# Performance work log

Hardware: AMD Instinct MI355X
Metric: run time of the kernel (lower is better)

## Reference

```python
import jax, jax.numpy as jnp
import numpy as np


def setup_inputs() -> dict:
    key = jax.random.key(0)
    ks = jax.random.split(key, 6)
    b, t, s, qu, vu, d = 8, 64, 512, 512, 512, 512
    return {
        "query": jax.random.normal(ks[0], (b, t, qu), jnp.float32),
        "value": jax.random.normal(ks[1], (b, s, vu), jnp.float32),
        "mask": jax.random.randint(ks[2], (b, s), 0, 2).astype(bool),
        "W1_w": jax.random.normal(ks[3], (qu, d), jnp.float32) * (1.0 / np.sqrt(qu)),
        "W1_b": jnp.zeros((d,), jnp.float32),
        "W2_w": jax.random.normal(ks[4], (vu, d), jnp.float32) * (1.0 / np.sqrt(vu)),
        "W2_b": jnp.zeros((d,), jnp.float32),
        "scale": jax.random.normal(ks[5], (d,), jnp.float32) * 0.05,
    }


def reference(query, value, mask, W1_w, W1_b, W2_w, W2_b, scale):
    # Dense projections
    q = jnp.einsum('btq,qd->btd', query, W1_w) + W1_b   # [b,t,d]
    k = jnp.einsum('bsv,vd->bsd', value, W2_w) + W2_b   # [b,s,d]
    # Additive (Bahdanau) score with learned scale vector (Keras use_scale=True)
    # scores[b,t,s] = sum_d scale[d] * tanh(q[b,t,d] + k[b,s,d])
    scores = jnp.einsum('btsd,d->bts', jnp.tanh(q[:, :, None, :] + k[:, None, :, :]), scale)
    # Mask over source positions (value mask); query mask is all-ones (no-op)
    scores = jnp.where(mask[:, None, :], scores, jnp.float32(-1e9))
    attention_weights = jax.nn.softmax(scores, axis=-1)   # [b,t,s]
    context_vector = jnp.einsum('bts,bsv->btv', attention_weights, value)  # [b,t,vu]
    return context_vector, attention_weights
```

## Files before the change

### kernel.cpp

```cpp
#include <hip/hip_runtime.h>
#include <hip/hip_bf16.h>
#include <hip/hip_fp16.h>

#define B_  8
#define T_  64
#define S_  512
#define D_  512

#define QN (512 * 512)
#define KN (4096 * 512)

#define TLOG2E 2.8853900817779268f
#define LOG2E  1.4426950408889634f

typedef __attribute__((ext_vector_type(8))) short bf16x8;
typedef __attribute__((ext_vector_type(4))) float f32x4;

__device__ __forceinline__ unsigned int pk2(float a, float b) {
    float2 f; f.x = a; f.y = b;
    __hip_bfloat162 h = __float22bfloat162_rn(f);
    return *(unsigned int*)&h;
}
__device__ __forceinline__ unsigned int pkh(float a, float b) {
    __half2 h = __floats2half2_rn(a, b);
    return *(unsigned int*)&h;
}
__device__ __forceinline__ float2 up2(unsigned int u) {
    __half2 h = *(__half2*)&u;
    return __half22float2(h);
}

__global__ __launch_bounds__(256) void mfma_gemm(
    const float* __restrict__ query, const float* __restrict__ value,
    const float* __restrict__ W1, const float* __restrict__ W2,
    const float* __restrict__ b1, const float* __restrict__ b2,
    float* __restrict__ qproj, unsigned short* __restrict__ kTb,
    unsigned short* __restrict__ vh)
{
    __shared__ __align__(16) unsigned short Ab[2][64][72];
    __shared__ __align__(16) unsigned short Bs[2][64][72];

    const int x = blockIdx.x;
    const int tid  = threadIdx.x;

    if (x >= 576) {
        const int c = x - 576;
        const float* src = value + (size_t)c * 128 * 512;
        unsigned short* dst = vh + (size_t)c * 128 * 512;
#pragma unroll 4
        for (int i = 0; i < 64; ++i) {
            const int f = i * 256 + tid;
            float4 v4 = *(const float4*)(src + (size_t)f * 4);
            uint2 o; o.x = pkh(v4.x, v4.y); o.y = pkh(v4.z, v4.w);
            *(uint2*)(dst + (size_t)f * 4) = o;
        }
        return;
    }

    const float *A, *W;
    int tm, tn;
    bool isq;
    if (x < 512) {
        tm = (x & 7) * 8 + ((x >> 3) & 7);
        tn = x >> 6;
        A = value; W = W2; isq = false;
    } else {
        int r = x - 512;
        tm = r >> 3; tn = r & 7;
        A = query; W = W1; isq = true;
    }

    const int lane = tid & 63;
    const int wid  = tid >> 6;
    const int wm = (wid & 1) * 32, wn = (wid >> 1) * 32;
    const int fm = lane & 15, fq = lane >> 4;

    f32x4 acc00 = {0.f, 0.f, 0.f, 0.f};
    f32x4 acc01 = acc00, acc10 = acc00, acc11 = acc00;

    const int ar = tid >> 2;
    const int kc = (tid & 3) * 16;
    const float* Ag = A + (size_t)(tm * 64 + ar) * 512 + kc;
    const int c0 = (tid & 15) * 4;
    const int kp = (tid >> 4) * 2;
    const float* Wg = W + (size_t)kp * 512 + tn * 64 + c0;

    float4 av0, av1, av2, av3;
    float4 wv0, wv1, wv2, wv3;

#define LOADT(KOFF) do {                                                      \
        av0 = *(const float4*)(Ag + (KOFF));                                  \
        av1 = *(const float4*)(Ag + (KOFF) + 4);                              \
        av2 = *(const float4*)(Ag + (KOFF) + 8);                              \
        av3 = *(const float4*)(Ag + (KOFF) + 12);                             \
        wv0 = *(const float4*)(Wg + (size_t)(KOFF) * 512);                    \
        wv1 = *(const float4*)(Wg + (size_t)(KOFF) * 512 + 512);              \
        wv2 = *(const float4*)(Wg + (size_t)((KOFF) + 32) * 512);             \
        wv3 = *(const float4*)(Wg + (size_t)((KOFF) + 32) * 512 + 512);       \
    } while (0)

#define STAGE(BUF) do {                                                       \
        uint4 p0, p1;                                                         \
        p0.x = pk2(av0.x, av0.y); p0.y = pk2(av0.z, av0.w);                   \
        p0.z = pk2(av1.x, av1.y); p0.w = pk2(av1.z, av1.w);                   \
        p1.x = pk2(av2.x, av2.y); p1.y = pk2(av2.z, av2.w);                   \
        p1.z = pk2(av3.x, av3.y); p1.w = pk2(av3.z, av3.w);                   \
        *(uint4*)&Ab[BUF][ar][kc]     = p0;                                   \
        *(uint4*)&Ab[BUF][ar][kc + 8] = p1;                                   \
        *(unsigned int*)&Bs[BUF][c0 + 0][kp]      = pk2(wv0.x, wv1.x);        \
        *(unsigned int*)&Bs[BUF][c0 + 1][kp]      = pk2(wv0.y, wv1.y);        \
        *(unsigned int*)&Bs[BUF][c0 + 2][kp]      = pk2(wv0.z, wv1.z);        \
        *(unsigned int*)&Bs[BUF][c0 + 3][kp]      = pk2(wv0.w, wv1.w);        \
        *(unsigned int*)&Bs[BUF][c0 + 0][kp + 32] = pk2(wv2.x, wv3.x);        \
        *(unsigned int*)&Bs[BUF][c0 + 1][kp + 32] = pk2(wv2.y, wv3.y);        \
        *(unsigned int*)&Bs[BUF][c0 + 2][kp + 32] = pk2(wv2.z, wv3.z);        \
        *(unsigned int*)&Bs[BUF][c0 + 3][kp + 32] = pk2(wv2.w, wv3.w);        \
    } while (0)

    LOADT(0);
    STAGE(0);
    LOADT(64);
    __syncthreads();

    for (int i = 0; i < 8; ++i) {
        const int cur = i & 1, nxt = cur ^ 1;
        bf16x8 a0, a1, b0, b1v;
#pragma unroll
        for (int kk = 0; kk < 64; kk += 32) {
            a0  = *(const bf16x8*)&Ab[cur][wm + fm][kk + fq * 8];
            a1  = *(const bf16x8*)&Ab[cur][wm + 16 + fm][kk + fq * 8];
            b0  = *(const bf16x8*)&Bs[cur][wn + fm][kk + fq * 8];
            b1v = *(const bf16x8*)&Bs[cur][wn + 16 + fm][kk + fq * 8];
            acc00 = __builtin_amdgcn_mfma_f32_16x16x32_bf16(a0, b0,  acc00, 0, 0, 0);
            acc01 = __builtin_amdgcn_mfma_f32_16x16x32_bf16(a0, b1v, acc01, 0, 0, 0);
            acc10 = __builtin_amdgcn_mfma_f32_16x16x32_bf16(a1, b0,  acc10, 0, 0, 0);
            acc11 = __builtin_amdgcn_mfma_f32_16x16x32_bf16(a1, b1v, acc11, 0, 0, 0);
        }
        if (i < 7) {
            STAGE(nxt);
            const int kn = ((i + 2) & 7) * 64;
            LOADT(kn);
        }
        __syncthreads();
    }
#undef STAGE
#undef LOADT

    const int n0 = tn * 64 + wn + fm;
    const int n1 = n0 + 16;
    const int m0 = tm * 64 + wm + fq * 4;
    if (isq) {
        float bias0 = b1[n0] + b2[n0];
        float bias1 = b1[n1] + b2[n1];
#pragma unroll
        for (int r = 0; r < 4; ++r) {
            qproj[(size_t)(m0 + r) * 512 + n0]      = (acc00[r] + bias0) * TLOG2E;
            qproj[(size_t)(m0 + r) * 512 + n1]      = (acc01[r] + bias1) * TLOG2E;
            qproj[(size_t)(m0 + 16 + r) * 512 + n0] = (acc10[r] + bias0) * TLOG2E;
            qproj[(size_t)(m0 + 16 + r) * 512 + n1] = (acc11[r] + bias1) * TLOG2E;
        }
    } else {
        const int bb = m0 >> 9;
        const int sl = m0 & 511;
        unsigned short* kb = kTb + (size_t)(bb * 512) * 512;
#define EX2(V) __builtin_amdgcn_exp2f((V) * TLOG2E)
        uint2 o;
        o.x = pkh(EX2(acc00[0]), EX2(acc00[1]));
        o.y = pkh(EX2(acc00[2]), EX2(acc00[3]));
        *(uint2*)(kb + (size_t)n0 * 512 + sl) = o;
        o.x = pkh(EX2(acc10[0]), EX2(acc10[1]));
        o.y = pkh(EX2(acc10[2]), EX2(acc10[3]));
        *(uint2*)(kb + (size_t)n0 * 512 + sl + 16) = o;
        o.x = pkh(EX2(acc01[0]), EX2(acc01[1]));
        o.y = pkh(EX2(acc01[2]), EX2(acc01[3]));
        *(uint2*)(kb + (size_t)n1 * 512 + sl) = o;
        o.x = pkh(EX2(acc11[0]), EX2(acc11[1]));
        o.y = pkh(EX2(acc11[2]), EX2(acc11[3]));
        *(uint2*)(kb + (size_t)n1 * 512 + sl + 16) = o;
#undef EX2
    }
}

__global__ __launch_bounds__(1024) void fused_attn(
    const float* __restrict__ qproj, const unsigned short* __restrict__ kTb,
    const int*   __restrict__ mask,  const float* __restrict__ scale,
    const unsigned short* __restrict__ vh,
    float* __restrict__ ctx, float* __restrict__ attn)
{
    const int blk = blockIdx.x;
    const int b  = blk & 7;
    const int tp = blk >> 3;
    const size_t row0 = (size_t)(b * T_ + tp * 2);

    __shared__ __align__(16) float q0A[512];
    __shared__ __align__(16) float dA[512];
    __shared__ __align__(16) float cA[512];
    __shared__ __align__(16) float4 pex[4][256];
    __shared__ __align__(16) float4 part[2][8][128];
    __shared__ __align__(16) float2 wc[8][64];
    __shared__ int  sidc[8][64];
    __shared__ int  cntA[8];
    __shared__ float2 red2[16];

    const int tid  = threadIdx.x;
    const int lane = tid & 63;
    const int wid  = tid >> 6;

    if (tid < 512) {
        float q0v = qproj[row0 * D_ + tid];
        float q1v = qproj[(row0 + 1) * D_ + tid];
        q0A[tid] = __builtin_amdgcn_exp2f(q0v);
        dA[tid]  = __builtin_amdgcn_exp2f(q1v - q0v);
        cA[tid]  = scale[tid];
    }
    __syncthreads();

    const int sp  = tid & 255;
    const int dq  = tid >> 8;
    const int dlo = dq * 128;
    const unsigned short* kb = kTb + ((size_t)(b * 512 + dlo)) * 512 + sp * 2;

    float p00 = 0.f, p10 = 0.f, p01 = 0.f, p11 = 0.f;

    unsigned int nf0 = *(const unsigned int*)(kb);
    unsigned int nf1 = *(const unsigned int*)(kb + 512);
    unsigned int nf2 = *(const unsigned int*)(kb + 1024);
    unsigned int nf3 = *(const unsigned int*)(kb + 1536);

#define SC2(KU, EQ, DV, CV) do {                                              \
        float2 ek = up2(KU);                                                  \
        float e0 = (EQ) * ek.x;                                               \
        float ra = __builtin_amdgcn_rcpf(e0 + 1.0f);                          \
        float rb = __builtin_amdgcn_rcpf(fmaf(e0, (DV), 1.0f));               \
        p00 = fmaf((CV), ra, p00); p10 = fmaf((CV), rb, p10);                 \
        float e1 = (EQ) * ek.y;                                               \
        float rc = __builtin_amdgcn_rcpf(e1 + 1.0f);                          \
        float rd = __builtin_amdgcn_rcpf(fmaf(e1, (DV), 1.0f));               \
        p01 = fmaf((CV), rc, p01); p11 = fmaf((CV), rd, p11);                 \
    } while (0)

    for (int g = 0; g < 32; ++g) {
        unsigned int kf0 = nf0, kf1 = nf1, kf2 = nf2, kf3 = nf3;
        const unsigned short* nb = kb + (size_t)(((g + 1) & 31) * 4) * 512;
        nf0 = *(const unsigned int*)(nb);
        nf1 = *(const unsigned int*)(nb + 512);
        nf2 = *(const unsigned int*)(nb + 1024);
        nf3 = *(const unsigned int*)(nb + 1536);
        const int d0 = dlo + g * 4;
        float4 q4 = *(const float4*)&q0A[d0];
        float4 dl = *(const float4*)&dA[d0];
        float4 c4 = *(const float4*)&cA[d0];
        SC2(kf0, q4.x, dl.x, c4.x);
        SC2(kf1, q4.y, dl.y, c4.y);
        SC2(kf2, q4.z, dl.z, c4.z);
        SC2(kf3, q4.w, dl.w, c4.w);
    }
#undef SC2

    {
        float4 pq; pq.x = p00; pq.y = p10; pq.z = p01; pq.w = p11;
        pex[dq][sp] = pq;
    }
    __syncthreads();

    float e0 = 0.f, e1 = 0.f;
    int   m = 0, rank = 0;
    if (tid < 512) {
        const int s = tid;
        const int s2 = s >> 1;
        const bool odd = (s & 1) != 0;
        float4 r0 = pex[0][s2], r1 = pex[1][s2];
        float4 r2 = pex[2][s2], r3 = pex[3][s2];
        float pt0 = odd ? ((r0.z + r1.z) + (r2.z + r3.z))
                        : ((r0.x + r1.x) + (r2.x + r3.x));
        float pt1 = odd ? ((r0.w + r1.w) + (r2.w + r3.w))
                        : ((r0.y + r1.y) + (r2.y + r3.y));
        m = mask[b * S_ + s];
        if (m) {
            e0 = __builtin_amdgcn_exp2f(-TLOG2E * pt0);
            e1 = __builtin_amdgcn_exp2f(-TLOG2E * pt1);
        }
        unsigned long long bal = __ballot(m != 0);
        rank = __popcll(bal & ((1ull << lane) - 1ull));
        if (lane == 0) cntA[wid] = (int)__popcll(bal);
        if (m) sidc[wid][rank] = lane;
        float2 sm; sm.x = e0; sm.y = e1;
#pragma unroll
        for (int off = 32; off >= 1; off >>= 1) {
            sm.x += __shfl_xor(sm.x, off);
            sm.y += __shfl_xor(sm.y, off);
        }
        if (lane == 0) red2[wid] = sm;
    }
    __syncthreads();

    if (tid < 512) {
        const int s = tid;
        float2 SS = red2[0];
#pragma unroll
        for (int i = 1; i < 8; ++i) {
            SS.x += red2[i].x;
            SS.y += red2[i].y;
        }
        const float w0 = e0 * __builtin_amdgcn_rcpf(SS.x);
        const float w1 = e1 * __builtin_amdgcn_rcpf(SS.y);
        if (m) {
            float2 wpair; wpair.x = w0; wpair.y = w1;
            wc[wid][rank] = wpair;
        }
        attn[row0 * S_ + s]       = w0;
        attn[(row0 + 1) * S_ + s] = w1;
    }
    __syncthreads();

    const int g  = tid >> 7;
    const int v4 = tid & 127;
    const unsigned short* vbase = vh + ((size_t)(b * S_) + g * 64) * D_ + v4 * 4;
    float4 a0; a0.x = 0.f; a0.y = 0.f; a0.z = 0.f; a0.w = 0.f;
    float4 a1 = a0;

    const int cnt = cntA[g];
    float2 w0r, w1r; uint2 u0r, u1r;
    w0r.x = 0.f; w0r.y = 0.f; w1r = w0r;
    u0r.x = 0u; u0r.y = 0u; u1r = u0r;
    if (0 < cnt) {
        int so = sidc[g][0]; w0r = wc[g][0];
        u0r = *(const uint2*)(vbase + (size_t)so * D_);
    }
    if (1 < cnt) {
        int so = sidc[g][1]; w1r = wc[g][1];
        u1r = *(const uint2*)(vbase + (size_t)so * D_);
    }
    for (int r = 0; r < cnt; ++r) {
        float2 w = w0r; uint2 u = u0r;
        w0r = w1r; u0r = u1r;
        if (r + 2 < cnt) {
            int so = sidc[g][r + 2]; w1r = wc[g][r + 2];
            u1r = *(const uint2*)(vbase + (size_t)so * D_);
        }
        float2 lo = up2(u.x), hi = up2(u.y);
        a0.x = fmaf(w.x, lo.x, a0.x); a0.y = fmaf(w.x, lo.y, a0.y);
        a0.z = fmaf(w.x, hi.x, a0.z); a0.w = fmaf(w.x, hi.y, a0.w);
        a1.x = fmaf(w.y, lo.x, a1.x); a1.y = fmaf(w.y, lo.y, a1.y);
        a1.z = fmaf(w.y, hi.x, a1.z); a1.w = fmaf(w.y, hi.y, a1.w);
    }
    part[0][g][v4] = a0;
    part[1][g][v4] = a1;
    __syncthreads();
    if (tid < 256) {
        const int t = tid >> 7, v = tid & 127;
        float4 o; o.x = 0.f; o.y = 0.f; o.z = 0.f; o.w = 0.f;
#pragma unroll
        for (int gg = 0; gg < 8; ++gg) {
            float4 p = part[t][gg][v];
            o.x += p.x; o.y += p.y; o.z += p.z; o.w += p.w;
        }
        *(float4*)(ctx + (row0 + t) * D_ + v * 4) = o;
    }
}

extern "C" void kernel_launch(void* const* d_in, const int* in_sizes, int n_in,
                              void* d_out, int out_size, void* d_ws, size_t ws_size,
                              hipStream_t stream) {
    const float* query = (const float*)d_in[0];
    const float* value = (const float*)d_in[1];
    const int*   mask  = (const int*)  d_in[2];
    const float* W1w   = (const float*)d_in[3];
    const float* W1b   = (const float*)d_in[4];
    const float* W2w   = (const float*)d_in[5];
    const float* W2b   = (const float*)d_in[6];
    const float* scale = (const float*)d_in[7];

    float* ctx  = (float*)d_out;
    float* attn = (float*)d_out + (size_t)B_ * T_ * D_;

    float* qproj = (float*)d_ws;
    unsigned short* kTb = (unsigned short*)(qproj + (size_t)QN);
    unsigned short* vh  = kTb + (size_t)KN;

    mfma_gemm<<<608, 256, 0, stream>>>(query, value, W1w, W2w, W1b, W2b,
                                       qproj, kTb, vh);
    fused_attn<<<256, 1024, 0, stream>>>(qproj, kTb, mask, scale, vh,
                                         ctx, attn);
}
```

Measured before the change: 125.5 us.

## Compact masked source positions before score computation to skip masked tanh work

The kernel now builds a compacted list of unmasked source indices at the start of each block and evaluates the additive tanh score only for those positions. Masked positions previously paid the full D-loop cost before being discarded. Work per block drops roughly in proportion to the mask density. In exchange, K loads become scattered 16-bit gathers instead of coalesced 32-bit pair loads. The context reduction is also rebalanced so the compacted entries are split evenly across wave groups, and masked attention outputs are written as zero directly.

```diff
diff --git a/kernel.cpp b/kernel.cpp
--- a/kernel.cpp
+++ b/kernel.cpp
@@ -197,93 +197,119 @@
     __shared__ __align__(16) float cA[512];
     __shared__ __align__(16) float4 pex[4][256];
     __shared__ __align__(16) float4 part[2][8][128];
-    __shared__ __align__(16) float2 wc[8][64];
-    __shared__ int  sidc[8][64];
-    __shared__ int  cntA[8];
+    __shared__ __align__(16) float2 wc[512];
+    __shared__ int  sidc[512];
+    __shared__ int  mA[512];
+    __shared__ int  wcnt[8];
+    __shared__ int  cntS;
     __shared__ float2 red2[16];
 
     const int tid  = threadIdx.x;
     const int lane = tid & 63;
     const int wid  = tid >> 6;
 
+    int m = 0, rank = 0;
     if (tid < 512) {
         float q0v = qproj[row0 * D_ + tid];
         float q1v = qproj[(row0 + 1) * D_ + tid];
         q0A[tid] = __builtin_amdgcn_exp2f(q0v);
         dA[tid]  = __builtin_amdgcn_exp2f(q1v - q0v);
         cA[tid]  = scale[tid];
-    }
-    __syncthreads();
-
-    const int sp  = tid & 255;
+        m = mask[b * S_ + tid];
+        mA[tid] = m;
+        unsigned long long bal = __ballot(m != 0);
+        rank = __popcll(bal & ((1ull << lane) - 1ull));
+        if (lane == 0) wcnt[wid] = (int)__popcll(bal);
+    }
+    __syncthreads();
+    if (tid < 512) {
+        int off = 0;
+#pragma unroll
+        for (int i = 0; i < 8; ++i) off += (i < wid) ? wcnt[i] : 0;
+        if (m) sidc[off + rank] = tid;
+        if (tid == 0) {
+            int tot = 0;
+#pragma unroll
+            for (int i = 0; i < 8; ++i) tot += wcnt[i];
+            cntS = tot;
+        }
+    }
+    __syncthreads();
+    const int cnt = cntS;
+    if (tid >= cnt && tid < 512) sidc[tid] = sidc[0];
+    __syncthreads();
+
+    const int cp  = tid & 255;
     const int dq  = tid >> 8;
     const int dlo = dq * 128;
-    const unsigned short* kb = kTb + ((size_t)(b * 512 + dlo)) * 512 + sp * 2;
 
     float p00 = 0.f, p10 = 0.f, p01 = 0.f, p11 = 0.f;
 
-    unsigned int nf0 = *(const unsigned int*)(kb);
-    unsigned int nf1 = *(const unsigned int*)(kb + 512);
-    unsigned int nf2 = *(const unsigned int*)(kb + 1024);
-    unsigned int nf3 = *(const unsigned int*)(kb + 1536);
-
-#define SC2(KU, EQ, DV, CV) do {                                              \
-        float2 ek = up2(KU);                                                  \
-        float e0 = (EQ) * ek.x;                                               \
-        float ra = __builtin_amdgcn_rcpf(e0 + 1.0f);                          \
-        float rb = __builtin_amdgcn_rcpf(fmaf(e0, (DV), 1.0f));               \
+    if (2 * cp < cnt) {
+        const int s0 = sidc[2 * cp];
+        const int s1 = sidc[2 * cp + 1];
+        const unsigned short* kbase = kTb + ((size_t)(b * 512 + dlo)) * 512;
+        const unsigned short* kb0 = kbase + s0;
+        const unsigned short* kb1 = kbase + s1;
+
+        unsigned short n00, n01, n02, n03, n10, n11, n12, n13;
+        n00 = kb0[0]; n01 = kb0[512]; n02 = kb0[1024]; n03 = kb0[1536];
+        n10 = kb1[0]; n11 = kb1[512]; n12 = kb1[1024]; n13 = kb1[1536];
+
+#define SC1(U0, U1, EQ, DV, CV) do {                                          \
+        float ek0 = __half2float(*(const __half*)&(U0));                      \
+        float e0s = (EQ) * ek0;                                               \
+        float ra = __builtin_amdgcn_rcpf(e0s + 1.0f);                         \
+        float rb = __builtin_amdgcn_rcpf(fmaf(e0s, (DV), 1.0f));              \
         p00 = fmaf((CV), ra, p00); p10 = fmaf((CV), rb, p10);                 \
-        float e1 = (EQ) * ek.y;                                               \
-        float rc = __builtin_amdgcn_rcpf(e1 + 1.0f);                          \
-        float rd = __builtin_amdgcn_rcpf(fmaf(e1, (DV), 1.0f));               \
+        float ek1 = __half2float(*(const __half*)&(U1));                      \
+        float e1s = (EQ) * ek1;                                               \
+        float rc = __builtin_amdgcn_rcpf(e1s + 1.0f);                         \
+        float rd = __builtin_amdgcn_rcpf(fmaf(e1s, (DV), 1.0f));              \
         p01 = fmaf((CV), rc, p01); p11 = fmaf((CV), rd, p11);                 \
     } while (0)
 
-    for (int g = 0; g < 32; ++g) {
-        unsigned int kf0 = nf0, kf1 = nf1, kf2 = nf2, kf3 = nf3;
-        const unsigned short* nb = kb + (size_t)(((g + 1) & 31) * 4) * 512;
-        nf0 = *(const unsigned int*)(nb);
-        nf1 = *(const unsigned int*)(nb + 512);
-        nf2 = *(const unsigned int*)(nb + 1024);
-        nf3 = *(const unsigned int*)(nb + 1536);
-        const int d0 = dlo + g * 4;
-        float4 q4 = *(const float4*)&q0A[d0];
-        float4 dl = *(const float4*)&dA[d0];
-        float4 c4 = *(const float4*)&cA[d0];
-        SC2(kf0, q4.x, dl.x, c4.x);
-        SC2(kf1, q4.y, dl.y, c4.y);
-        SC2(kf2, q4.z, dl.z, c4.z);
-        SC2(kf3, q4.w, dl.w, c4.w);
-    }
-#undef SC2
+        for (int g = 0; g < 32; ++g) {
+            unsigned short c00 = n00, c01 = n01, c02 = n02, c03 = n03;
+            unsigned short c10 = n10, c11 = n11, c12 = n12, c13 = n13;
+            const size_t gn = (size_t)(((g + 1) & 31) * 4) * 512;
+            const unsigned short* nb0 = kb0 + gn;
+            const unsigned short* nb1 = kb1 + gn;
+            n00 = nb0[0]; n01 = nb0[512]; n02 = nb0[1024]; n03 = nb0[1536];
+            n10 = nb1[0]; n11 = nb1[512]; n12 = nb1[1024]; n13 = nb1[1536];
+            const int d0 = dlo + g * 4;
+            float4 q4 = *(const float4*)&q0A[d0];
+            float4 dl = *(const float4*)&dA[d0];
+            float4 c4 = *(const float4*)&cA[d0];
+            SC1(c00, c10, q4.x, dl.x, c4.x);
+            SC1(c01, c11, q4.y, dl.y, c4.y);
+            SC1(c02, c12, q4.z, dl.z, c4.z);
+            SC1(c03, c13, q4.w, dl.w, c4.w);
+        }
+#undef SC1
+    }
 
     {
         float4 pq; pq.x = p00; pq.y = p10; pq.z = p01; pq.w = p11;
-        pex[dq][sp] = pq;
+        pex[dq][cp] = pq;
     }
     __syncthreads();
 
     float e0 = 0.f, e1 = 0.f;
-    int   m = 0, rank = 0;
     if (tid < 512) {
-        const int s = tid;
-        const int s2 = s >> 1;
-        const bool odd = (s & 1) != 0;
-        float4 r0 = pex[0][s2], r1 = pex[1][s2];
-        float4 r2 = pex[2][s2], r3 = pex[3][s2];
+        const int c = tid;
+        const int cp2 = c >> 1;
+        const bool odd = (c & 1) != 0;
+        float4 r0 = pex[0][cp2], r1 = pex[1][cp2];
+        float4 r2 = pex[2][cp2], r3 = pex[3][cp2];
         float pt0 = odd ? ((r0.z + r1.z) + (r2.z + r3.z))
                         : ((r0.x + r1.x) + (r2.x + r3.x));
         float pt1 = odd ? ((r0.w + r1.w) + (r2.w + r3.w))
                         : ((r0.y + r1.y) + (r2.y + r3.y));
-        m = mask[b * S_ + s];
-        if (m) {
+        if (c < cnt) {
             e0 = __builtin_amdgcn_exp2f(-TLOG2E * pt0);
             e1 = __builtin_amdgcn_exp2f(-TLOG2E * pt1);
         }
-        unsigned long long bal = __ballot(m != 0);
-        rank = __popcll(bal & ((1ull << lane) - 1ull));
-        if (lane == 0) cntA[wid] = (int)__popcll(bal);
-        if (m) sidc[wid][rank] = lane;
         float2 sm; sm.x = e0; sm.y = e1;
 #pragma unroll
         for (int off = 32; off >= 1; off >>= 1) {
@@ -295,7 +321,7 @@
     __syncthreads();
 
     if (tid < 512) {
-        const int s = tid;
+        const int c = tid;
         float2 SS = red2[0];
 #pragma unroll
         for (int i = 1; i < 8; ++i) {
@@ -304,39 +330,45 @@
         }
         const float w0 = e0 * __builtin_amdgcn_rcpf(SS.x);
         const float w1 = e1 * __builtin_amdgcn_rcpf(SS.y);
-        if (m) {
+        if (c < cnt) {
+            const int so = sidc[c];
             float2 wpair; wpair.x = w0; wpair.y = w1;
-            wc[wid][rank] = wpair;
-        }
-        attn[row0 * S_ + s]       = w0;
-        attn[(row0 + 1) * S_ + s] = w1;
+            wc[c] = wpair;
+            attn[row0 * S_ + so]       = w0;
+            attn[(row0 + 1) * S_ + so] = w1;
+        }
+        if (!mA[tid]) {
+            attn[row0 * S_ + tid]       = 0.f;
+            attn[(row0 + 1) * S_ + tid] = 0.f;
+        }
     }
     __syncthreads();
 
     const int g  = tid >> 7;
     const int v4 = tid & 127;
-    const unsigned short* vbase = vh + ((size_t)(b * S_) + g * 64) * D_ + v4 * 4;
+    const unsigned short* vb = vh + (size_t)(b * S_) * D_ + v4 * 4;
     float4 a0; a0.x = 0.f; a0.y = 0.f; a0.z = 0.f; a0.w = 0.f;
     float4 a1 = a0;
 
-    const int cnt = cntA[g];
+    const int trips = (cnt > g) ? ((cnt - 1 - g) >> 3) + 1 : 0;
     float2 w0r, w1r; uint2 u0r, u1r;
     w0r.x = 0.f; w0r.y = 0.f; w1r = w0r;
     u0r.x = 0u; u0r.y = 0u; u1r = u0r;
-    if (0 < cnt) {
-        int so = sidc[g][0]; w0r = wc[g][0];
-        u0r = *(const uint2*)(vbase + (size_t)so * D_);
-    }
-    if (1 < cnt) {
-        int so = sidc[g][1]; w1r = wc[g][1];
-        u1r = *(const uint2*)(vbase + (size_t)so * D_);
-    }
-    for (int r = 0; r < cnt; ++r) {
+    if (0 < trips) {
+        w0r = wc[g];
+        u0r = *(const uint2*)(vb + (size_t)sidc[g] * D_);
+    }
+    if (1 < trips) {
+        w1r = wc[g + 8];
+        u1r = *(const uint2*)(vb + (size_t)sidc[g + 8] * D_);
+    }
+    for (int r = 0; r < trips; ++r) {
         float2 w = w0r; uint2 u = u0r;
         w0r = w1r; u0r = u1r;
-        if (r + 2 < cnt) {
-            int so = sidc[g][r + 2]; w1r = wc[g][r + 2];
-            u1r = *(const uint2*)(vbase + (size_t)so * D_);
+        if (r + 2 < trips) {
+            const int c = g + 8 * (r + 2);
+            w1r = wc[c];
+            u1r = *(const uint2*)(vb + (size_t)sidc[c] * D_);
         }
         float2 lo = up2(u.x), hi = up2(u.y);
         a0.x = fmaf(w.x, lo.x, a0.x); a0.y = fmaf(w.x, lo.y, a0.y);
```

After: 124.8 us. Within noise of the previous version (-0.5%).
